# Kernel optimization log

Hardware: AMD Instinct MI355X
Metric: run time of the kernel (lower is better)

The kernel has to match this reference:

```python
import jax, jax.numpy as jnp
import numpy as np

N = 96          # nodes == feature dim == d_model
T = 160         # number of dFC time frames
D = 96          # dim_in / d_model
D_STATE = 64
D_CONV = 4
HEADDIM = 32
NGROUPS = 6
D_INNER = 2 * D               # expand=2 -> 192
NHEADS = D_INNER // HEADDIM   # 6
EMB = 24
DOUT = 64
D_IN_PROJ = 2 * D_INNER + 2 * NGROUPS * D_STATE + NHEADS  # 1158
CONV_DIM = D_INNER + 2 * NGROUPS * D_STATE                 # 960
BN_EPS = 1e-5
RMS_EPS = 1e-5


def _mamba2(z, in_proj, conv_w, conv_b, dt_bias, A_log, Dparam, norm_w, out_proj):
    # z: (b, L, D)
    b, L, _ = z.shape
    zxbcdt = z @ in_proj                               # (b, L, D_IN_PROJ)
    zg = zxbcdt[..., :D_INNER]                         # gate branch
    xBC = zxbcdt[..., D_INNER:D_INNER + CONV_DIM]
    dt = jax.nn.softplus(zxbcdt[..., -NHEADS:] + dt_bias)  # (b, L, H)
    # causal depthwise conv1d (kernel D_CONV) + SiLU
    xp = jnp.pad(xBC, ((0, 0), (D_CONV - 1, 0), (0, 0)))
    xc = conv_b + sum(xp[:, k:k + L, :] * conv_w[:, k] for k in range(D_CONV))
    xc = jax.nn.silu(xc)
    x = xc[..., :D_INNER].reshape(b, L, NHEADS, HEADDIM)
    Bm = xc[..., D_INNER:D_INNER + NGROUPS * D_STATE].reshape(b, L, NGROUPS, D_STATE)
    Cm = xc[..., D_INNER + NGROUPS * D_STATE:].reshape(b, L, NGROUPS, D_STATE)
    # nheads == ngroups -> one head per group
    A = -jnp.exp(A_log)                                # (H,)

    def step(state, inp):
        xt, Bt, Ct, dtt = inp                          # (b,h,p),(b,h,n),(b,h,n),(b,h)
        dA = jnp.exp(dtt * A)                          # (b,h)
        state = state * dA[..., None, None] + (dtt[..., None, None] * xt[..., None]) * Bt[:, :, None, :]
        y = jnp.einsum('bhpn,bhn->bhp', state, Ct) + Dparam[None, :, None] * xt
        return state, y

    init = jnp.zeros((b, NHEADS, HEADDIM, D_STATE), z.dtype)
    seq = (jnp.swapaxes(x, 0, 1), jnp.swapaxes(Bm, 0, 1), jnp.swapaxes(Cm, 0, 1), jnp.swapaxes(dt, 0, 1))
    _, ys = jax.lax.scan(step, init, seq)              # (L, b, h, p)
    y = jnp.swapaxes(ys, 0, 1).reshape(b, L, D_INNER)
    # gated RMSNorm (norm_before_gate=False): rmsnorm(y * silu(z)) * w
    yg = y * jax.nn.silu(zg)
    yg = yg * jax.lax.rsqrt(jnp.mean(yg * yg, axis=-1, keepdims=True) + RMS_EPS) * norm_w
    return yg @ out_proj


def _forward(input, hem, subnet, gine_w1, gine_b1, gine_w2, gine_b2, bn_w, bn_b,
             hem_emb, subnet_emb, in_proj, conv_w, conv_b, dt_bias, A_log, Dparam,
             norm_w, out_proj, out_fc_w, out_fc_b, mu_w, mu_b, sigma_w, sigma_b):
    xs = jnp.swapaxes(input, 0, 1)                     # (T, N, D): node feats per frame
    # per-node meta embedding, edge_attr[j,i] = concat(a[j], a[i]) with a = [hem_emb, subnet_emb]
    a = jnp.concatenate([hem_emb[hem], subnet_emb[subnet]], axis=-1)   # (N, 48)
    H2 = 2 * EMB
    # GINE aggregation over dense graph: agg[t,i] = sum_j relu(x[t,j] + e[j,i])
    # first 48 channels depend only on source j -> collapses to one vector per t
    s1 = jnp.sum(jax.nn.relu(xs[:, :, :H2] + a[None, :, :]), axis=1)   # (T, 48)
    # last 48 channels depend on source feat and target meta
    m2 = jax.nn.relu(xs[:, :, None, H2:] + a[None, None, :, :])        # (T, Nj, Ni, 48)
    s2 = jnp.sum(m2, axis=1)                                           # (T, N, 48)
    agg = jnp.concatenate([jnp.broadcast_to(s1[:, None, :], s2.shape), s2], axis=-1)
    gin = xs + agg                                     # (1+eps)*x + agg, eps=0
    h = jax.nn.relu(gin @ gine_w1 + gine_b1) @ gine_w2 + gine_b2
    h = h + xs                                         # residual (dropout = eval identity)
    # BatchNorm1d per frame over the node axis (biased variance)
    mu_n = jnp.mean(h, axis=1, keepdims=True)
    var_n = jnp.mean((h - mu_n) ** 2, axis=1, keepdims=True)
    h = (h - mu_n) * jax.lax.rsqrt(var_n + BN_EPS) * bn_w + bn_b
    z = jnp.swapaxes(h, 0, 1)                          # (N, T, D): nodes are the batch
    e = _mamba2(z, in_proj, conv_w, conv_b, dt_bias, A_log, Dparam, norm_w, out_proj)
    e = jnp.mean(e, axis=1)                            # (N, D)
    x1 = jax.nn.elu(jnp.tanh(e @ out_fc_w + out_fc_b))
    mu = x1 @ mu_w + mu_b
    sigma = jax.nn.elu(x1 @ sigma_w + sigma_b) + 1.0 + 1e-14
    return x1, mu, sigma


def setup_inputs() -> dict:
    key = jax.random.key(0)
    ks = jax.random.split(key, 16)
    rn = lambda k, s, sc: jax.random.normal(k, s, jnp.float32) * sc
    return {
        'input': jax.random.normal(ks[0], (N, T, N), jnp.float32),
        'hem': jax.random.randint(ks[1], (N,), 0, 2),
        'subnet': jax.random.randint(ks[2], (N,), 0, 17),
        'gine_w1': rn(ks[3], (D, D), 0.1), 'gine_b1': jnp.zeros((D,), jnp.float32),
        'gine_w2': rn(ks[4], (D, D), 0.1), 'gine_b2': jnp.zeros((D,), jnp.float32),
        'bn_w': jnp.ones((D,), jnp.float32), 'bn_b': jnp.zeros((D,), jnp.float32),
        'hem_emb': rn(ks[5], (2, EMB), 0.5), 'subnet_emb': rn(ks[6], (17, EMB), 0.5),
        'in_proj': rn(ks[7], (D, D_IN_PROJ), 0.05),
        'conv_w': rn(ks[8], (CONV_DIM, D_CONV), 0.2),
        'conv_b': jnp.zeros((CONV_DIM,), jnp.float32),
        'dt_bias': rn(ks[9], (NHEADS,), 0.1),
        'A_log': jnp.log(jnp.arange(1, NHEADS + 1, dtype=jnp.float32)),
        'Dparam': jnp.ones((NHEADS,), jnp.float32),
        'norm_w': jnp.ones((D_INNER,), jnp.float32),
        'out_proj': rn(ks[10], (D_INNER, D), 0.05),
        'out_fc_w': rn(ks[11], (D, D), 0.1), 'out_fc_b': jnp.zeros((D,), jnp.float32),
        'mu_w': rn(ks[12], (D, DOUT), 0.1), 'mu_b': jnp.zeros((DOUT,), jnp.float32),
        'sigma_w': rn(ks[13], (D, DOUT), 0.1), 'sigma_b': jnp.zeros((DOUT,), jnp.float32),
    }


def reference(input, hem, subnet, gine_w1, gine_b1, gine_w2, gine_b2, bn_w, bn_b,
              hem_emb, subnet_emb, in_proj, conv_w, conv_b, dt_bias, A_log, Dparam,
              norm_w, out_proj, out_fc_w, out_fc_b, mu_w, mu_b, sigma_w, sigma_b):
    return _forward(input, hem, subnet, gine_w1, gine_b1, gine_w2, gine_b2, bn_w, bn_b,
                    hem_emb, subnet_emb, in_proj, conv_w, conv_b, dt_bias, A_log, Dparam,
                    norm_w, out_proj, out_fc_w, out_fc_b, mu_w, mu_b, sigma_w, sigma_b)
```

## Files before the change

kernel.cpp:

```cpp
#include <hip/hip_runtime.h>
#include <hip/hip_bf16.h>
#include <math.h>

#define NB 96
#define TT 160
#define DD 96
#define D_STATE 64
#define D_CONV 4
#define HEADDIM 32
#define NGROUPS 6
#define D_INNER 192
#define NHEADS 6
#define EMB 24
#define DOUT 64
#define D_IN_PROJ 1158
#define CONV_DIM 960
#define TN 15360
#define BN_EPS 1e-5f
#define RMS_EPS 1e-5f

typedef __attribute__((ext_vector_type(8))) short short8;
typedef __attribute__((ext_vector_type(4))) float f32x4;

__device__ __forceinline__ float siluf(float x) { return x / (1.f + expf(-x)); }
__device__ __forceinline__ float softplusf(float x) {
    return fmaxf(x, 0.f) + log1pf(expf(-fabsf(x)));
}
__device__ __forceinline__ unsigned short bf16r(float x) {
  union { __hip_bfloat16 h; unsigned short u; } cv;
  cv.h = __float2bfloat16(x);
  return cv.u;
}
__device__ __forceinline__ unsigned int pack_bf2(float a, float b) {
  return (unsigned int)bf16r(a) | ((unsigned int)bf16r(b) << 16);
}
__device__ __forceinline__ float bf16f(unsigned short u) {
  return __uint_as_float((unsigned int)u << 16);
}

__global__ __launch_bounds__(256) void k1_agg(
    const float* __restrict__ input, const int* __restrict__ hem,
    const int* __restrict__ subnet, const float* __restrict__ hem_emb,
    const float* __restrict__ subnet_emb, float* __restrict__ gin) {
  int t = blockIdx.x;
  __shared__ float xs[96 * 96];
  __shared__ float al[96 * 48];
  __shared__ float s1[48];
  __shared__ float s2[96 * 48];
  int tid = threadIdx.x;

  for (int o = tid; o < 96 * 96; o += 256) {
    int i = o / 96, d = o % 96;
    xs[o] = input[i * TN + t * 96 + d];
  }
  for (int o = tid; o < 96 * 48; o += 256) {
    int i = o / 48, c = o % 48;
    al[o] = (c < 24) ? hem_emb[hem[i] * 24 + c]
                     : subnet_emb[subnet[i] * 24 + (c - 24)];
  }
  __syncthreads();
  if (tid < 48) {
    float s = 0.f;
    for (int i = 0; i < 96; i++) s += fmaxf(xs[i * 96 + tid] + al[i * 48 + tid], 0.f);
    s1[tid] = s;
  }
  for (int o = tid; o < 96 * 48; o += 256) {
    int j = o / 48, c = o % 48;
    float av = al[j * 48 + c];
    float s = 0.f;
    for (int i = 0; i < 96; i++) s += fmaxf(xs[i * 96 + 48 + c] + av, 0.f);
    s2[o] = s;
  }
  __syncthreads();
  for (int o = tid; o < 96 * 96; o += 256) {
    int j = o / 96, d = o % 96;
    float aggv = (d < 48) ? s1[d] : s2[j * 48 + (d - 48)];
    gin[t * 9216 + o] = xs[o] + aggv;
  }
}

__global__ __launch_bounds__(256) void k2_mlp(
    const float* __restrict__ gin, const float* __restrict__ input,
    const float* __restrict__ W1, const float* __restrict__ b1,
    const float* __restrict__ W2, const float* __restrict__ b2,
    float* __restrict__ H) {
  int r0 = blockIdx.x * 64;
  __shared__ float As[64][97];
  __shared__ float Bs[96][96];
  __shared__ float Hd[64][97];
  int tid = threadIdx.x;
  int tx = tid & 15, ty = tid >> 4;
  int c0 = tx * 6;
  int rb = ty * 4;

  for (int o = tid; o < 64 * 96; o += 256) As[o / 96][o % 96] = gin[(size_t)r0 * 96 + o];
  for (int o = tid; o < 96 * 96; o += 256) ((float*)Bs)[o] = W1[o];
  __syncthreads();

  float acc[4][6];
#pragma unroll
  for (int i = 0; i < 4; i++)
#pragma unroll
    for (int j = 0; j < 6; j++) acc[i][j] = b1[c0 + j];

#pragma unroll 4
  for (int k = 0; k < 96; k++) {
    float a0 = As[rb + 0][k], a1 = As[rb + 1][k], a2 = As[rb + 2][k], a3 = As[rb + 3][k];
    float b[6];
#pragma unroll
    for (int j = 0; j < 6; j++) b[j] = Bs[k][c0 + j];
#pragma unroll
    for (int j = 0; j < 6; j++) {
      acc[0][j] += a0 * b[j];
      acc[1][j] += a1 * b[j];
      acc[2][j] += a2 * b[j];
      acc[3][j] += a3 * b[j];
    }
  }
#pragma unroll
  for (int i = 0; i < 4; i++)
#pragma unroll
    for (int j = 0; j < 6; j++) Hd[rb + i][c0 + j] = fmaxf(acc[i][j], 0.f);
  __syncthreads();
  for (int o = tid; o < 96 * 96; o += 256) ((float*)Bs)[o] = W2[o];
#pragma unroll
  for (int i = 0; i < 4; i++)
#pragma unroll
    for (int j = 0; j < 6; j++) acc[i][j] = b2[c0 + j];
  __syncthreads();

#pragma unroll 4
  for (int k = 0; k < 96; k++) {
    float a0 = Hd[rb + 0][k], a1 = Hd[rb + 1][k], a2 = Hd[rb + 2][k], a3 = Hd[rb + 3][k];
    float b[6];
#pragma unroll
    for (int j = 0; j < 6; j++) b[j] = Bs[k][c0 + j];
#pragma unroll
    for (int j = 0; j < 6; j++) {
      acc[0][j] += a0 * b[j];
      acc[1][j] += a1 * b[j];
      acc[2][j] += a2 * b[j];
      acc[3][j] += a3 * b[j];
    }
  }
#pragma unroll
  for (int i = 0; i < 4; i++) {
    int r = r0 + rb + i;
    int t = r / 96, jn = r % 96;
    const float* resr = input + (size_t)jn * TN + t * 96 + c0;
#pragma unroll
    for (int j = 0; j < 6; j++)
      H[(size_t)r * 96 + c0 + j] = acc[i][j] + resr[j];
  }
}

__global__ __launch_bounds__(256) void k2_bn(
    const float* __restrict__ H, const float* __restrict__ bn_w,
    const float* __restrict__ bn_b, float* __restrict__ z) {
  int t = blockIdx.x;
  __shared__ float h[96 * 96];
  __shared__ float mu[96], rs[96];
  int tid = threadIdx.x;

  for (int o = tid; o < 9216; o += 256) h[o] = H[(size_t)t * 9216 + o];
  __syncthreads();
  if (tid < 96) {
    float m = 0.f;
    for (int j = 0; j < 96; j++) m += h[j * 96 + tid];
    m *= (1.f / 96.f);
    float v = 0.f;
    for (int j = 0; j < 96; j++) { float dd = h[j * 96 + tid] - m; v += dd * dd; }
    v *= (1.f / 96.f);
    mu[tid] = m;
    rs[tid] = rsqrtf(v + BN_EPS);
  }
  __syncthreads();
  for (int o = tid; o < 9216; o += 256) {
    int j = o / 96, d = o % 96;
    z[(size_t)j * TN + t * 96 + d] = (h[o] - mu[d]) * rs[d] * bn_w[d] + bn_b[d];
  }
}

__global__ __launch_bounds__(256) void k_convW(
    const float* __restrict__ ip, unsigned short* __restrict__ WT) {
  int idx = blockIdx.x * 256 + threadIdx.x;
  if (idx < 96 * D_IN_PROJ) {
    int k = idx / D_IN_PROJ, n = idx - k * D_IN_PROJ;
    WT[(size_t)n * 96 + k] = bf16r(ip[idx]);
  }
}

__global__ __launch_bounds__(256) void k3_mfma(
    const float* __restrict__ Z, const unsigned short* __restrict__ WT,
    float* __restrict__ C) {
  int m0 = blockIdx.x * 128;
  int n0 = blockIdx.y * 64;
  __shared__ unsigned short As[128][104];
  __shared__ unsigned short Bs[64][104];
  int tid = threadIdx.x;
  int lane = tid & 63, w = tid >> 6;

  for (int o = tid; o < 128 * 24; o += 256) {
    int r = o / 24, c4 = (o % 24) * 4;
    float4 v = *(const float4*)&Z[(size_t)(m0 + r) * 96 + c4];
    unsigned int p0 = pack_bf2(v.x, v.y);
    unsigned int p1 = pack_bf2(v.z, v.w);
    *(uint2*)&As[r][c4] = make_uint2(p0, p1);
  }
  for (int o = tid; o < 64 * 12; o += 256) {
    int nr = o / 12, seg = (o % 12) * 8;
    int n = n0 + nr;
    short8 v = {};
    if (n < D_IN_PROJ) v = *(const short8*)&WT[(size_t)n * 96 + seg];
    *(short8*)&Bs[nr][seg] = v;
  }
  __syncthreads();

  int q = lane >> 4, r16 = lane & 15;
  int wm = w * 32;
  f32x4 acc[2][4] = {};

#pragma unroll
  for (int ks = 0; ks < 3; ks++) {
    int k0 = ks * 32 + q * 8;
    short8 a0 = *(const short8*)&As[wm + r16][k0];
    short8 a1 = *(const short8*)&As[wm + 16 + r16][k0];
    short8 b0 = *(const short8*)&Bs[r16][k0];
    short8 b1 = *(const short8*)&Bs[16 + r16][k0];
    short8 b2 = *(const short8*)&Bs[32 + r16][k0];
    short8 b3 = *(const short8*)&Bs[48 + r16][k0];
    acc[0][0] = __builtin_amdgcn_mfma_f32_16x16x32_bf16(a0, b0, acc[0][0], 0, 0, 0);
    acc[0][1] = __builtin_amdgcn_mfma_f32_16x16x32_bf16(a0, b1, acc[0][1], 0, 0, 0);
    acc[0][2] = __builtin_amdgcn_mfma_f32_16x16x32_bf16(a0, b2, acc[0][2], 0, 0, 0);
    acc[0][3] = __builtin_amdgcn_mfma_f32_16x16x32_bf16(a0, b3, acc[0][3], 0, 0, 0);
    acc[1][0] = __builtin_amdgcn_mfma_f32_16x16x32_bf16(a1, b0, acc[1][0], 0, 0, 0);
    acc[1][1] = __builtin_amdgcn_mfma_f32_16x16x32_bf16(a1, b1, acc[1][1], 0, 0, 0);
    acc[1][2] = __builtin_amdgcn_mfma_f32_16x16x32_bf16(a1, b2, acc[1][2], 0, 0, 0);
    acc[1][3] = __builtin_amdgcn_mfma_f32_16x16x32_bf16(a1, b3, acc[1][3], 0, 0, 0);
  }

#pragma unroll
  for (int mf = 0; mf < 2; mf++) {
#pragma unroll
    for (int nf = 0; nf < 4; nf++) {
      int col = n0 + nf * 16 + r16;
      if (col < D_IN_PROJ) {
        int rowb = m0 + wm + mf * 16 + q * 4;
#pragma unroll
        for (int reg = 0; reg < 4; reg++)
          C[(size_t)(rowb + reg) * D_IN_PROJ + col] = acc[mf][nf][reg];
      }
    }
  }
}

__global__ __launch_bounds__(320) void k5_fused(
    const float* __restrict__ zx, const float* __restrict__ conv_w,
    const float* __restrict__ conv_b, const float* __restrict__ dt_bias,
    const float* __restrict__ A_log, const float* __restrict__ Dparam,
    float* __restrict__ y) {
  int b = blockIdx.x;
  int h = blockIdx.y;
  int tid = threadIdx.x;

  __shared__ __align__(16) unsigned char smem[67840];
  unsigned short* XdA = (unsigned short*)smem;
  unsigned short* Bb = (unsigned short*)(smem + 10240);
  unsigned short* Cb = (unsigned short*)(smem + 33280);
  unsigned short* xb = (unsigned short*)(smem + 56320);
  float* dt_s = (float*)(smem + 66560);
  float* sc_a = (float*)(smem + 67200);

  float Ah = -expf(A_log[h]);
  float Dh = Dparam[h];
  float dtb = dt_bias[h];
  const float* zrow = zx + (size_t)b * 160 * D_IN_PROJ;

  int cc = tid % 160, thalf = tid / 160;
  {
    int c, csrc;
    if (cc < 32) {
      c = h * 32 + cc;
      csrc = 192 + h * 32 + cc;
    } else if (cc < 96) {
      c = 192 + h * 64 + (cc - 32);
      csrc = 384 + h * 64 + (cc - 32);
    } else {
      c = 576 + h * 64 + (cc - 96);
      csrc = 768 + h * 64 + (cc - 96);
    }
    float cw0 = conv_w[c * 4 + 0], cw1 = conv_w[c * 4 + 1];
    float cw2 = conv_w[c * 4 + 2], cw3 = conv_w[c * 4 + 3];
    float cb = conv_b[c];
    unsigned short* cdst;
    int cstride;
    if (cc < 32)      { cdst = xb + cc;        cstride = 32; }
    else if (cc < 96) { cdst = Bb + (cc - 32); cstride = 72; }
    else              { cdst = Cb + (cc - 96); cstride = 72; }

    float rdt = 0.f;
    if (tid < 160) rdt = zrow[(size_t)tid * D_IN_PROJ + 1152 + h];

    int t0 = thalf * 80;
    float h0 = 0.f, h1 = 0.f, h2 = 0.f;
    if (thalf == 1) {
      h0 = zrow[(size_t)(t0 - 3) * D_IN_PROJ + csrc];
      h1 = zrow[(size_t)(t0 - 2) * D_IN_PROJ + csrc];
      h2 = zrow[(size_t)(t0 - 1) * D_IN_PROJ + csrc];
    }
#pragma unroll 8
    for (int i = 0; i < 80; i++) {
      int t = t0 + i;
      float d = zrow[(size_t)t * D_IN_PROJ + csrc];
      float o = cb + h0 * cw0 + h1 * cw1 + h2 * cw2 + d * cw3;
      cdst[t * cstride] = bf16r(siluf(o));
      h0 = h1; h1 = h2; h2 = d;
    }
    if (tid < 160) {
      float dtv = softplusf(rdt + dtb);
      dt_s[tid] = dtv;
      sc_a[tid] = dtv * Ah;
    }
  }
  __syncthreads();

  if (tid >= 64) {
    for (int i = tid - 64; i < 5120; i += 256) {
      int tau = i >> 5, p = i & 31;
      float xv = bf16f(xb[tau * 32 + p]);
      unsigned short v = bf16r(dt_s[tau] * xv);
      int t32 = tau & 31, K = tau >> 5;
      int hi = t32 >> 4, qq = (t32 & 15) >> 2, j = (t32 & 3) + 4 * hi;
      XdA[(((K * 4 + qq) << 5) + p) * 8 + j] = v;
    }
  } else {
    int l = tid;
    float a = sc_a[l];
    float bseg = sc_a[64 + l];
    float cseg = (l < 32) ? sc_a[128 + l] : 0.f;
#pragma unroll
    for (int off = 1; off < 64; off <<= 1) {
      float u = __shfl_up(a, off);
      if (l >= off) a += u;
    }
    float s0 = __shfl(a, 63);
#pragma unroll
    for (int off = 1; off < 64; off <<= 1) {
      float u = __shfl_up(bseg, off);
      if (l >= off) bseg += u;
    }
    bseg += s0;
    float s1 = __shfl(bseg, 63);
#pragma unroll
    for (int off = 1; off < 32; off <<= 1) {
      float u = __shfl_up(cseg, off);
      if (l >= off) cseg += u;
    }
    cseg += s1;
    sc_a[l] = a;
    sc_a[64 + l] = bseg;
    if (l < 32) sc_a[128 + l] = cseg;
  }
  __syncthreads();
  const float* lc = sc_a;

  int wid = tid >> 6, lane = tid & 63;
  int q = lane >> 4, r16 = lane & 15;
  int tbase = wid * 32;

  short8 cfr[2][2];
  float lct[2];
#pragma unroll
  for (int ft = 0; ft < 2; ft++) {
    int t = tbase + ft * 16 + r16;
    cfr[ft][0] = *(const short8*)&Cb[t * 72 + q * 8];
    cfr[ft][1] = *(const short8*)&Cb[t * 72 + 32 + q * 8];
    lct[ft] = lc[t];
  }
  f32x4 yacc[2][2] = {};

  for (int K = 0; K <= wid; K++) {
    short8 bfr[2][2];
    f32x4 lc4[2];
#pragma unroll
    for (int i = 0; i < 2; i++) {
      int tr = (2 * K + i) * 16 + r16;
      bfr[i][0] = *(const short8*)&Bb[tr * 72 + q * 8];
      bfr[i][1] = *(const short8*)&Bb[tr * 72 + 32 + q * 8];
      lc4[i] = *(const f32x4*)&lc[(2 * K + i) * 16 + q * 4];
    }
    f32x4 g[2][2] = {};
#pragma unroll
    for (int i = 0; i < 2; i++)
#pragma unroll
      for (int ft = 0; ft < 2; ft++) {
        g[i][ft] = __builtin_amdgcn_mfma_f32_16x16x32_bf16(bfr[i][0], cfr[ft][0], g[i][ft], 0, 0, 0);
        g[i][ft] = __builtin_amdgcn_mfma_f32_16x16x32_bf16(bfr[i][1], cfr[ft][1], g[i][ft], 0, 0, 0);
      }
#pragma unroll
    for (int i = 0; i < 2; i++)
#pragma unroll
      for (int ft = 0; ft < 2; ft++) {
        int t = tbase + ft * 16 + r16;
#pragma unroll
        for (int reg = 0; reg < 4; reg++) {
          int tau = 32 * K + i * 16 + q * 4 + reg;
          float w = (tau <= t) ? __expf(lct[ft] - lc4[i][reg]) : 0.f;
          g[i][ft][reg] *= w;
        }
      }
    short8 xfr[2];
#pragma unroll
    for (int mf = 0; mf < 2; mf++)
      xfr[mf] = *(const short8*)&XdA[(((K * 4 + q) << 5) + mf * 16 + r16) * 8];
#pragma unroll
    for (int ft = 0; ft < 2; ft++) {
      union { short8 s; unsigned int u[4]; } sb;
      sb.u[0] = pack_bf2(g[0][ft][0], g[0][ft][1]);
      sb.u[1] = pack_bf2(g[0][ft][2], g[0][ft][3]);
      sb.u[2] = pack_bf2(g[1][ft][0], g[1][ft][1]);
      sb.u[3] = pack_bf2(g[1][ft][2], g[1][ft][3]);
#pragma unroll
      for (int mf = 0; mf < 2; mf++)
        yacc[mf][ft] = __builtin_amdgcn_mfma_f32_16x16x32_bf16(xfr[mf], sb.s, yacc[mf][ft], 0, 0, 0);
    }
  }

#pragma unroll
  for (int mf = 0; mf < 2; mf++)
#pragma unroll
    for (int ft = 0; ft < 2; ft++) {
      int t = tbase + ft * 16 + r16;
      int p0 = mf * 16 + q * 4;
      float4 o;
      float* op = (float*)&o;
#pragma unroll
      for (int reg = 0; reg < 4; reg++) {
        float xv = bf16f(xb[t * 32 + p0 + reg]);
        op[reg] = yacc[mf][ft][reg] + Dh * xv;
      }
      *(float4*)&y[((size_t)(b * 160 + t)) * D_INNER + h * 32 + p0] = o;
    }
}

#define K6T 16

__global__ __launch_bounds__(256) void k6_head(
    const float* __restrict__ y, const float* __restrict__ zx,
    const float* __restrict__ norm_w, const float* __restrict__ out_proj,
    float* __restrict__ e_part) {
  int b = blockIdx.x;
  int ch = blockIdx.y;
  int tid = threadIdx.x;
  __shared__ float g[K6T][200];
  __shared__ float rf[K6T];
  __shared__ float nw[192];
  __shared__ float ep[K6T][97];
  int t0 = ch * K6T;

  if (tid < 192) nw[tid] = norm_w[tid];

  for (int v = tid; v < K6T * 48; v += 256) {
    int tt = v / 48, c4 = (v % 48) * 4;
    size_t row = (size_t)(b * 160 + t0 + tt);
    float4 yv = *(const float4*)&y[row * D_INNER + c4];
    float4 zg = *(const float4*)&zx[row * D_IN_PROJ + c4];
    float4 gv;
    gv.x = yv.x * siluf(zg.x);
    gv.y = yv.y * siluf(zg.y);
    gv.z = yv.z * siluf(zg.z);
    gv.w = yv.w * siluf(zg.w);
    *(float4*)&g[tt][c4] = gv;
  }
  __syncthreads();

  {
    int tt = tid >> 4, l = tid & 15;
    float ss = 0.f;
    for (int k = l; k < 192; k += 16) {
      float v = g[tt][k];
      ss += v * v;
    }
    ss += __shfl_xor(ss, 1);
    ss += __shfl_xor(ss, 2);
    ss += __shfl_xor(ss, 4);
    ss += __shfl_xor(ss, 8);
    if (l == 0) rf[tt] = rsqrtf(ss * (1.f / 192.f) + RMS_EPS);
  }
  __syncthreads();

  for (int v = tid; v < K6T * 48; v += 256) {
    int tt = v / 48, c4 = (v % 48) * 4;
    float rr = rf[tt];
    float4 gv = *(float4*)&g[tt][c4];
    gv.x *= rr * nw[c4 + 0];
    gv.y *= rr * nw[c4 + 1];
    gv.z *= rr * nw[c4 + 2];
    gv.w *= rr * nw[c4 + 3];
    *(float4*)&g[tt][c4] = gv;
  }
  __syncthreads();

  if (tid < 192) {
    int tt = tid & 15, grp = tid >> 4;
    int d0 = grp * 8;
    float acc[8] = {};
    for (int k = 0; k < 192; k++) {
      float gk = g[tt][k];
      float4 wv0 = *(const float4*)&out_proj[(size_t)k * 96 + d0];
      float4 wv1 = *(const float4*)&out_proj[(size_t)k * 96 + d0 + 4];
      acc[0] += gk * wv0.x;
      acc[1] += gk * wv0.y;
      acc[2] += gk * wv0.z;
      acc[3] += gk * wv0.w;
      acc[4] += gk * wv1.x;
      acc[5] += gk * wv1.y;
      acc[6] += gk * wv1.z;
      acc[7] += gk * wv1.w;
    }
#pragma unroll
    for (int j = 0; j < 8; j++) ep[tt][d0 + j] = acc[j];
  }
  __syncthreads();

  if (tid < 96) {
    float sum = 0.f;
#pragma unroll
    for (int tt = 0; tt < K6T; tt++) sum += ep[tt][tid];
    e_part[(size_t)ch * 9216 + b * 96 + tid] = sum;
  }
}

__global__ __launch_bounds__(128) void k7_out(
    const float* __restrict__ e_part, const float* __restrict__ fcw,
    const float* __restrict__ fcb, const float* __restrict__ mu_w,
    const float* __restrict__ mu_b, const float* __restrict__ sg_w,
    const float* __restrict__ sg_b, float* __restrict__ out) {
  int b = blockIdx.x;
  int tid = threadIdx.x;
  __shared__ float em[96];
  __shared__ float x1[96];
  if (tid < 96) {
    float s = 0.f;
    for (int c = 0; c < 10; c++) s += e_part[(size_t)c * 9216 + b * 96 + tid];
    em[tid] = s * (1.f / 160.f);
  }
  __syncthreads();
  if (tid < 96) {
    float acc = fcb[tid];
    for (int k = 0; k < 96; k++) acc += em[k] * fcw[k * 96 + tid];
    float tv = tanhf(acc);
    float ev = (tv > 0.f) ? tv : expm1f(tv);
    x1[tid] = ev;
    out[b * 96 + tid] = ev;
  }
  __syncthreads();
  int j = tid & 63, which = tid >> 6;
  if (which == 0) {
    float acc = mu_b[j];
    for (int k = 0; k < 96; k++) acc += x1[k] * mu_w[k * 64 + j];
    out[9216 + b * 64 + j] = acc;
  } else {
    float acc = sg_b[j];
    for (int k = 0; k < 96; k++) acc += x1[k] * sg_w[k * 64 + j];
    float ev = (acc > 0.f) ? acc : expm1f(acc);
    out[9216 + 6144 + b * 64 + j] = ev + 1.f + 1e-14f;
  }
}

extern "C" void kernel_launch(void* const* d_in, const int* in_sizes, int n_in,
                              void* d_out, int out_size, void* d_ws,
                              size_t ws_size, hipStream_t stream) {
  const float* input      = (const float*)d_in[0];
  const int*   hem        = (const int*)d_in[1];
  const int*   subnet     = (const int*)d_in[2];
  const float* gine_w1    = (const float*)d_in[3];
  const float* gine_b1    = (const float*)d_in[4];
  const float* gine_w2    = (const float*)d_in[5];
  const float* gine_b2    = (const float*)d_in[6];
  const float* bn_w       = (const float*)d_in[7];
  const float* bn_b       = (const float*)d_in[8];
  const float* hem_emb    = (const float*)d_in[9];
  const float* subnet_emb = (const float*)d_in[10];
  const float* in_proj    = (const float*)d_in[11];
  const float* conv_w     = (const float*)d_in[12];
  const float* conv_b     = (const float*)d_in[13];
  const float* dt_bias    = (const float*)d_in[14];
  const float* A_log      = (const float*)d_in[15];
  const float* Dparam     = (const float*)d_in[16];
  const float* norm_w     = (const float*)d_in[17];
  const float* out_proj   = (const float*)d_in[18];
  const float* out_fc_w   = (const float*)d_in[19];
  const float* out_fc_b   = (const float*)d_in[20];
  const float* mu_w       = (const float*)d_in[21];
  const float* mu_b       = (const float*)d_in[22];
  const float* sigma_w    = (const float*)d_in[23];
  const float* sigma_b    = (const float*)d_in[24];

  float* ws = (float*)d_ws;
  float* gin    = ws;
  float* z      = gin + 1474560;
  float* zx     = z + 1474560;
  float* y      = zx + 17786880;
  float* e_part = y + 2949120;
  unsigned short* WT = (unsigned short*)(y + 2893536);
  float* outp = (float*)d_out;

  k_convW<<<435, 256, 0, stream>>>(in_proj, WT);
  k1_agg<<<160, 256, 0, stream>>>(input, hem, subnet, hem_emb, subnet_emb, gin);
  k2_mlp<<<240, 256, 0, stream>>>(gin, input, gine_w1, gine_b1, gine_w2,
                                  gine_b2, gin);
  k2_bn<<<160, 256, 0, stream>>>(gin, bn_w, bn_b, z);
  k3_mfma<<<dim3(120, 19), 256, 0, stream>>>(z, WT, zx);
  k5_fused<<<dim3(96, 6), 320, 0, stream>>>(zx, conv_w, conv_b, dt_bias,
                                            A_log, Dparam, y);
  k6_head<<<dim3(96, 10), 256, 0, stream>>>(y, zx, norm_w, out_proj, e_part);
  k7_out<<<96, 128, 0, stream>>>(e_part, out_fc_w, out_fc_b, mu_w, mu_b,
                                 sigma_w, sigma_b, outp);
}
```

Before: 183.5 us.

## Store in_proj output as bf16 and double k5 thread count

```diff
diff --git a/kernel.cpp b/kernel.cpp
--- a/kernel.cpp
+++ b/kernel.cpp
@@ -14,6 +14,7 @@
 #define EMB 24
 #define DOUT 64
 #define D_IN_PROJ 1158
+#define ZXW_LD 1160
 #define CONV_DIM 960
 #define TN 15360
 #define BN_EPS 1e-5f
@@ -192,11 +193,12 @@
 
 __global__ __launch_bounds__(256) void k3_mfma(
     const float* __restrict__ Z, const unsigned short* __restrict__ WT,
-    float* __restrict__ C) {
+    unsigned short* __restrict__ zxw, float* __restrict__ dtw) {
   int m0 = blockIdx.x * 128;
   int n0 = blockIdx.y * 64;
   __shared__ unsigned short As[128][104];
   __shared__ unsigned short Bs[64][104];
+  unsigned short* Cs = &As[0][0];
   int tid = threadIdx.x;
   int lane = tid & 63, w = tid >> 6;
 
@@ -239,26 +241,37 @@
     acc[1][3] = __builtin_amdgcn_mfma_f32_16x16x32_bf16(a1, b3, acc[1][3], 0, 0, 0);
   }
 
+  __syncthreads();
+
 #pragma unroll
   for (int mf = 0; mf < 2; mf++) {
 #pragma unroll
     for (int nf = 0; nf < 4; nf++) {
       int col = n0 + nf * 16 + r16;
-      if (col < D_IN_PROJ) {
-        int rowb = m0 + wm + mf * 16 + q * 4;
-#pragma unroll
-        for (int reg = 0; reg < 4; reg++)
-          C[(size_t)(rowb + reg) * D_IN_PROJ + col] = acc[mf][nf][reg];
+      int rowb = wm + mf * 16 + q * 4;
+#pragma unroll
+      for (int reg = 0; reg < 4; reg++) {
+        Cs[(rowb + reg) * 64 + nf * 16 + r16] = bf16r(acc[mf][nf][reg]);
+        if (col >= 1152 && col < D_IN_PROJ)
+          dtw[(size_t)(m0 + rowb + reg) * 6 + (col - 1152)] = acc[mf][nf][reg];
       }
     }
   }
-}
-
-__global__ __launch_bounds__(320) void k5_fused(
-    const float* __restrict__ zx, const float* __restrict__ conv_w,
-    const float* __restrict__ conv_b, const float* __restrict__ dt_bias,
-    const float* __restrict__ A_log, const float* __restrict__ Dparam,
-    float* __restrict__ y) {
+  __syncthreads();
+
+  for (int v = tid; v < 1024; v += 256) {
+    int r = v >> 3, seg = (v & 7) * 8;
+    if (n0 + seg + 8 <= ZXW_LD)
+      *(short8*)&zxw[(size_t)(m0 + r) * ZXW_LD + n0 + seg] =
+          *(const short8*)&Cs[r * 64 + seg];
+  }
+}
+
+__global__ __launch_bounds__(640) void k5_fused(
+    const unsigned short* __restrict__ zxw, const float* __restrict__ dtw,
+    const float* __restrict__ conv_w, const float* __restrict__ conv_b,
+    const float* __restrict__ dt_bias, const float* __restrict__ A_log,
+    const float* __restrict__ Dparam, float* __restrict__ y) {
   int b = blockIdx.x;
   int h = blockIdx.y;
   int tid = threadIdx.x;
@@ -274,10 +287,10 @@
   float Ah = -expf(A_log[h]);
   float Dh = Dparam[h];
   float dtb = dt_bias[h];
-  const float* zrow = zx + (size_t)b * 160 * D_IN_PROJ;
-
-  int cc = tid % 160, thalf = tid / 160;
+  const unsigned short* zroww = zxw + (size_t)b * 160 * ZXW_LD;
+
   {
+    int cc = tid % 160, tq = tid / 160;
     int c, csrc;
     if (cc < 32) {
       c = h * 32 + cc;
@@ -299,19 +312,19 @@
     else              { cdst = Cb + (cc - 96); cstride = 72; }
 
     float rdt = 0.f;
-    if (tid < 160) rdt = zrow[(size_t)tid * D_IN_PROJ + 1152 + h];
-
-    int t0 = thalf * 80;
+    if (tid < 160) rdt = dtw[(size_t)(b * 160 + tid) * 6 + h];
+
+    int t0 = tq * 40;
     float h0 = 0.f, h1 = 0.f, h2 = 0.f;
-    if (thalf == 1) {
-      h0 = zrow[(size_t)(t0 - 3) * D_IN_PROJ + csrc];
-      h1 = zrow[(size_t)(t0 - 2) * D_IN_PROJ + csrc];
-      h2 = zrow[(size_t)(t0 - 1) * D_IN_PROJ + csrc];
+    if (tq > 0) {
+      h0 = bf16f(zroww[(size_t)(t0 - 3) * ZXW_LD + csrc]);
+      h1 = bf16f(zroww[(size_t)(t0 - 2) * ZXW_LD + csrc]);
+      h2 = bf16f(zroww[(size_t)(t0 - 1) * ZXW_LD + csrc]);
     }
 #pragma unroll 8
-    for (int i = 0; i < 80; i++) {
+    for (int i = 0; i < 40; i++) {
       int t = t0 + i;
-      float d = zrow[(size_t)t * D_IN_PROJ + csrc];
+      float d = bf16f(zroww[(size_t)t * ZXW_LD + csrc]);
       float o = cb + h0 * cw0 + h1 * cw1 + h2 * cw2 + d * cw3;
       cdst[t * cstride] = bf16r(siluf(o));
       h0 = h1; h1 = h2; h2 = d;
@@ -325,13 +338,15 @@
   __syncthreads();
 
   if (tid >= 64) {
-    for (int i = tid - 64; i < 5120; i += 256) {
-      int tau = i >> 5, p = i & 31;
-      float xv = bf16f(xb[tau * 32 + p]);
-      unsigned short v = bf16r(dt_s[tau] * xv);
-      int t32 = tau & 31, K = tau >> 5;
-      int hi = t32 >> 4, qq = (t32 & 15) >> 2, j = (t32 & 3) + 4 * hi;
-      XdA[(((K * 4 + qq) << 5) + p) * 8 + j] = v;
+    for (int row = tid - 64; row < 640; row += 576) {
+      int p = row & 31, qq = (row >> 5) & 3, K = row >> 7;
+      short8 v;
+#pragma unroll
+      for (int j = 0; j < 8; j++) {
+        int tau = K * 32 + (j & 3) + 4 * qq + 16 * (j >> 2);
+        ((unsigned short*)&v)[j] = bf16r(dt_s[tau] * bf16f(xb[tau * 32 + p]));
+      }
+      *(short8*)&XdA[row * 8] = v;
     }
   } else {
     int l = tid;
@@ -366,20 +381,16 @@
 
   int wid = tid >> 6, lane = tid & 63;
   int q = lane >> 4, r16 = lane & 15;
-  int tbase = wid * 32;
-
-  short8 cfr[2][2];
-  float lct[2];
-#pragma unroll
-  for (int ft = 0; ft < 2; ft++) {
-    int t = tbase + ft * 16 + r16;
-    cfr[ft][0] = *(const short8*)&Cb[t * 72 + q * 8];
-    cfr[ft][1] = *(const short8*)&Cb[t * 72 + 32 + q * 8];
-    lct[ft] = lc[t];
-  }
-  f32x4 yacc[2][2] = {};
-
-  for (int K = 0; K <= wid; K++) {
+  int tbase = wid * 16;
+  int t = tbase + r16;
+
+  short8 cfr0 = *(const short8*)&Cb[t * 72 + q * 8];
+  short8 cfr1 = *(const short8*)&Cb[t * 72 + 32 + q * 8];
+  float lct = lc[t];
+  f32x4 yacc[2] = {};
+  int Kmax = wid >> 1;
+
+  for (int K = 0; K <= Kmax; K++) {
     short8 bfr[2][2];
     f32x4 lc4[2];
 #pragma unroll
@@ -389,64 +400,53 @@
       bfr[i][1] = *(const short8*)&Bb[tr * 72 + 32 + q * 8];
       lc4[i] = *(const f32x4*)&lc[(2 * K + i) * 16 + q * 4];
     }
-    f32x4 g[2][2] = {};
-#pragma unroll
-    for (int i = 0; i < 2; i++)
-#pragma unroll
-      for (int ft = 0; ft < 2; ft++) {
-        g[i][ft] = __builtin_amdgcn_mfma_f32_16x16x32_bf16(bfr[i][0], cfr[ft][0], g[i][ft], 0, 0, 0);
-        g[i][ft] = __builtin_amdgcn_mfma_f32_16x16x32_bf16(bfr[i][1], cfr[ft][1], g[i][ft], 0, 0, 0);
+    f32x4 g[2] = {};
+#pragma unroll
+    for (int i = 0; i < 2; i++) {
+      g[i] = __builtin_amdgcn_mfma_f32_16x16x32_bf16(bfr[i][0], cfr0, g[i], 0, 0, 0);
+      g[i] = __builtin_amdgcn_mfma_f32_16x16x32_bf16(bfr[i][1], cfr1, g[i], 0, 0, 0);
+    }
+#pragma unroll
+    for (int i = 0; i < 2; i++) {
+#pragma unroll
+      for (int reg = 0; reg < 4; reg++) {
+        int tau = 32 * K + i * 16 + q * 4 + reg;
+        float w = (tau <= t) ? __expf(lct - lc4[i][reg]) : 0.f;
+        g[i][reg] *= w;
       }
-#pragma unroll
-    for (int i = 0; i < 2; i++)
-#pragma unroll
-      for (int ft = 0; ft < 2; ft++) {
-        int t = tbase + ft * 16 + r16;
-#pragma unroll
-        for (int reg = 0; reg < 4; reg++) {
-          int tau = 32 * K + i * 16 + q * 4 + reg;
-          float w = (tau <= t) ? __expf(lct[ft] - lc4[i][reg]) : 0.f;
-          g[i][ft][reg] *= w;
-        }
-      }
+    }
     short8 xfr[2];
 #pragma unroll
     for (int mf = 0; mf < 2; mf++)
       xfr[mf] = *(const short8*)&XdA[(((K * 4 + q) << 5) + mf * 16 + r16) * 8];
-#pragma unroll
-    for (int ft = 0; ft < 2; ft++) {
-      union { short8 s; unsigned int u[4]; } sb;
-      sb.u[0] = pack_bf2(g[0][ft][0], g[0][ft][1]);
-      sb.u[1] = pack_bf2(g[0][ft][2], g[0][ft][3]);
-      sb.u[2] = pack_bf2(g[1][ft][0], g[1][ft][1]);
-      sb.u[3] = pack_bf2(g[1][ft][2], g[1][ft][3]);
-#pragma unroll
-      for (int mf = 0; mf < 2; mf++)
-        yacc[mf][ft] = __builtin_amdgcn_mfma_f32_16x16x32_bf16(xfr[mf], sb.s, yacc[mf][ft], 0, 0, 0);
-    }
-  }
-
-#pragma unroll
-  for (int mf = 0; mf < 2; mf++)
-#pragma unroll
-    for (int ft = 0; ft < 2; ft++) {
-      int t = tbase + ft * 16 + r16;
-      int p0 = mf * 16 + q * 4;
-      float4 o;
-      float* op = (float*)&o;
-#pragma unroll
-      for (int reg = 0; reg < 4; reg++) {
-        float xv = bf16f(xb[t * 32 + p0 + reg]);
-        op[reg] = yacc[mf][ft][reg] + Dh * xv;
-      }
-      *(float4*)&y[((size_t)(b * 160 + t)) * D_INNER + h * 32 + p0] = o;
-    }
+    union { short8 s; unsigned int u[4]; } sb;
+    sb.u[0] = pack_bf2(g[0][0], g[0][1]);
+    sb.u[1] = pack_bf2(g[0][2], g[0][3]);
+    sb.u[2] = pack_bf2(g[1][0], g[1][1]);
+    sb.u[3] = pack_bf2(g[1][2], g[1][3]);
+#pragma unroll
+    for (int mf = 0; mf < 2; mf++)
+      yacc[mf] = __builtin_amdgcn_mfma_f32_16x16x32_bf16(xfr[mf], sb.s, yacc[mf], 0, 0, 0);
+  }
+
+#pragma unroll
+  for (int mf = 0; mf < 2; mf++) {
+    int p0 = mf * 16 + q * 4;
+    float4 o;
+    float* op = (float*)&o;
+#pragma unroll
+    for (int reg = 0; reg < 4; reg++) {
+      float xv = bf16f(xb[t * 32 + p0 + reg]);
+      op[reg] = yacc[mf][reg] + Dh * xv;
+    }
+    *(float4*)&y[((size_t)(b * 160 + t)) * D_INNER + h * 32 + p0] = o;
+  }
 }
 
 #define K6T 16
 
 __global__ __launch_bounds__(256) void k6_head(
-    const float* __restrict__ y, const float* __restrict__ zx,
+    const float* __restrict__ y, const unsigned short* __restrict__ zxw,
     const float* __restrict__ norm_w, const float* __restrict__ out_proj,
     float* __restrict__ e_part) {
   int b = blockIdx.x;
@@ -460,17 +460,20 @@
 
   if (tid < 192) nw[tid] = norm_w[tid];
 
-  for (int v = tid; v < K6T * 48; v += 256) {
-    int tt = v / 48, c4 = (v % 48) * 4;
+  for (int v = tid; v < K6T * 24; v += 256) {
+    int tt = v / 24, c8 = (v % 24) * 8;
     size_t row = (size_t)(b * 160 + t0 + tt);
-    float4 yv = *(const float4*)&y[row * D_INNER + c4];
-    float4 zg = *(const float4*)&zx[row * D_IN_PROJ + c4];
-    float4 gv;
-    gv.x = yv.x * siluf(zg.x);
-    gv.y = yv.y * siluf(zg.y);
-    gv.z = yv.z * siluf(zg.z);
-    gv.w = yv.w * siluf(zg.w);
-    *(float4*)&g[tt][c4] = gv;
+    short8 zg8 = *(const short8*)&zxw[row * ZXW_LD + c8];
+    float4 y0 = *(const float4*)&y[row * D_INNER + c8];
+    float4 y1 = *(const float4*)&y[row * D_INNER + c8 + 4];
+    float* yp0 = (float*)&y0;
+    float* yp1 = (float*)&y1;
+#pragma unroll
+    for (int k = 0; k < 4; k++)
+      g[tt][c8 + k] = yp0[k] * siluf(bf16f((unsigned short)zg8[k]));
+#pragma unroll
+    for (int k = 0; k < 4; k++)
+      g[tt][c8 + 4 + k] = yp1[k] * siluf(bf16f((unsigned short)zg8[4 + k]));
   }
   __syncthreads();
 
@@ -600,9 +603,11 @@
   float* ws = (float*)d_ws;
   float* gin    = ws;
   float* z      = gin + 1474560;
-  float* zx     = z + 1474560;
-  float* y      = zx + 17786880;
+  float* zxf    = z + 1474560;
+  float* y      = zxf + 17786880;
   float* e_part = y + 2949120;
+  float* dtw    = e_part + 92160;
+  unsigned short* zxw = (unsigned short*)zxf;
   unsigned short* WT = (unsigned short*)(y + 2893536);
   float* outp = (float*)d_out;
 
@@ -611,10 +616,10 @@
   k2_mlp<<<240, 256, 0, stream>>>(gin, input, gine_w1, gine_b1, gine_w2,
                                   gine_b2, gin);
   k2_bn<<<160, 256, 0, stream>>>(gin, bn_w, bn_b, z);
-  k3_mfma<<<dim3(120, 19), 256, 0, stream>>>(z, WT, zx);
-  k5_fused<<<dim3(96, 6), 320, 0, stream>>>(zx, conv_w, conv_b, dt_bias,
+  k3_mfma<<<dim3(120, 19), 256, 0, stream>>>(z, WT, zxw, dtw);
+  k5_fused<<<dim3(96, 6), 640, 0, stream>>>(zxw, dtw, conv_w, conv_b, dt_bias,
                                             A_log, Dparam, y);
-  k6_head<<<dim3(96, 10), 256, 0, stream>>>(y, zx, norm_w, out_proj, e_part);
+  k6_head<<<dim3(96, 10), 256, 0, stream>>>(y, zxw, norm_w, out_proj, e_part);
   k7_out<<<96, 128, 0, stream>>>(e_part, out_fc_w, out_fc_b, mu_w, mu_b,
                                  sigma_w, sigma_b, outp);
 }
```

Result: faster. 164.0 us (-10.6%).
